# Optimization experiments

Measured on AMD Instinct MI355X. Metric: run time of the kernel, lower is better.

## Reference

```python
import jax, jax.numpy as jnp
import numpy as np

IB = 8      # input/hidden activation bits
ABMVM = 8   # gate activation bits after MVM
ABNM = 8    # near-memory compute bits
NL = 0.05   # analog noise level
CY_DIV = 2.0
CY_SCALE = 2.0


def quant_pass(x, wb, sign):
    # Faithful port of QuantFunc.forward: clip/clamp then fake-quant (round to grid).
    if wb is None or wb == 0:
        return x
    if sign:
        delta = 0.0 if wb == 1 else 1.0 / (2.0 ** (wb - 1))
        x = jnp.clip(x, -1.0 + delta, 1.0 - delta)
    else:
        x = jnp.clip(x, 0.0, 1.0)
    if wb == 1:
        return jnp.sign(x)
    scale = 2.0 ** (wb - 1) if sign else 2.0 ** wb
    return jnp.round(x * scale) / scale


def setup_inputs() -> dict:
    key = jax.random.key(0)
    ks = jax.random.split(key, 7)
    B, I, H = 4096, 1024, 1024
    return {
        "input": jax.random.normal(ks[0], (B, I), jnp.float32),
        "hx": jax.random.normal(ks[1], (B, H), jnp.float32),
        "cx": jax.random.normal(ks[2], (B, H), jnp.float32),
        "weight_ih": jax.random.normal(ks[3], (4 * H, I), jnp.float32) * 0.1,
        "weight_hh": jax.random.normal(ks[4], (4 * H, H), jnp.float32) * 0.1,
        "bias_ih": jax.random.normal(ks[5], (4 * H,), jnp.float32) * 0.1,
        "bias_hh": jax.random.normal(ks[6], (4 * H,), jnp.float32) * 0.1,
        "train": 0,
    }


def reference(input, hx, cx, weight_ih, weight_hh, bias_ih, bias_hh, train):
    # Per-call Gaussian noise (simulated analog hardware); fixed key for reproducibility.
    nk = jax.random.split(jax.random.key(42), 4)
    noise_w_ih = jax.random.normal(nk[0], weight_ih.T.shape, weight_ih.dtype) * weight_ih.max() * NL
    noise_w_hh = jax.random.normal(nk[1], weight_hh.T.shape, weight_hh.dtype) * weight_hh.max() * NL
    noise_b_ih = jax.random.normal(nk[2], bias_ih.shape, bias_ih.dtype) * bias_ih.max() * NL
    noise_b_hh = jax.random.normal(nk[3], bias_hh.shape, bias_hh.dtype) * bias_hh.max() * NL

    # gates: [B, 4H]
    gates = (quant_pass(input, IB, True) @ (weight_ih.T + noise_w_ih) + bias_ih + noise_b_ih
             + quant_pass(hx, IB, True) @ (weight_hh.T + noise_w_hh) + bias_hh + noise_b_hh)

    ingate, forgetgate, cellgate, outgate = jnp.split(gates, 4, axis=1)
    ingate = quant_pass(jax.nn.sigmoid(ingate), ABMVM, False)
    forgetgate = quant_pass(jax.nn.sigmoid(forgetgate), ABMVM, False)
    cellgate = quant_pass(jnp.tanh(cellgate), ABMVM, True)
    outgate = quant_pass(jax.nn.sigmoid(outgate), ABMVM, False)

    cy = quant_pass((quant_pass(forgetgate * cx, ABNM, True)
                     + quant_pass(ingate * cellgate, ABNM, True)) / CY_DIV, ABNM, True)
    hy = quant_pass(outgate * quant_pass(jnp.tanh(cy * CY_SCALE), ABNM, True), ABNM, True)
    return (hy, cy)
```

## Files before the change

### kernel.cpp

```cpp
#include <hip/hip_runtime.h>
#include <hip/hip_bf16.h>
#include <stdint.h>
#include <stddef.h>


#define PART 1

typedef __attribute__((ext_vector_type(8))) short bf16x8;
typedef __attribute__((ext_vector_type(4))) float f32x4;

#define BATCH 4096

#define WS_A_OFF    ((size_t)0)
#define WS_B_OFF    ((size_t)16 << 20)
#define WS_BIAS_OFF ((size_t)48 << 20)
#define WS_MAX_OFF  (WS_BIAS_OFF + 16384)

__host__ __device__ inline void tf2x32(uint32_t k0, uint32_t k1,
                                       uint32_t x0, uint32_t x1,
                                       uint32_t &o0, uint32_t &o1)
{
  const uint32_t k2 = k0 ^ k1 ^ 0x1BD11BDAu;
#define TFR(r) { x0 += x1; x1 = (x1 << (r)) | (x1 >> (32 - (r))); x1 ^= x0; }
  x0 += k0; x1 += k1;
  TFR(13) TFR(15) TFR(26) TFR(6)
  x0 += k1; x1 += k2 + 1u;
  TFR(17) TFR(29) TFR(16) TFR(24)
  x0 += k2; x1 += k0 + 2u;
  TFR(13) TFR(15) TFR(26) TFR(6)
  x0 += k0; x1 += k1 + 3u;
  TFR(17) TFR(29) TFR(16) TFR(24)
  x0 += k1; x1 += k2 + 4u;
  TFR(13) TFR(15) TFR(26) TFR(6)
  x0 += k2; x1 += k0 + 5u;
#undef TFR
  o0 = x0; o1 = x1;
}

__device__ inline uint32_t jax_bits32(uint32_t k0, uint32_t k1, uint32_t i, uint32_t size)
{
#if PART
  uint32_t a, b;
  tf2x32(k0, k1, 0u, i, a, b);
  return a ^ b;
#else
  uint32_t half = size >> 1, a, b;
  if (i < half) { tf2x32(k0, k1, i, i + half, a, b); return a; }
  tf2x32(k0, k1, i - half, i, a, b); return b;
#endif
}

__device__ inline float bits_to_normal(uint32_t bits)
{
  float f = __uint_as_float((bits >> 9) | 0x3F800000u) - 1.0f;
  const float lo = -0x1.fffffep-1f;
  float u = fmaxf(lo, f * 2.0f + lo);
  float w = -log1pf(-u * u);
  float p;
  if (w < 5.0f) {
    w -= 2.5f;
    p = 2.81022636e-08f;
    p = fmaf(p, w, 3.43273939e-07f);
    p = fmaf(p, w, -3.5233877e-06f);
    p = fmaf(p, w, -4.39150654e-06f);
    p = fmaf(p, w, 0.00021858087f);
    p = fmaf(p, w, -0.00125372503f);
    p = fmaf(p, w, -0.00417768164f);
    p = fmaf(p, w, 0.246640727f);
    p = fmaf(p, w, 1.50140941f);
  } else {
    w = sqrtf(w) - 3.0f;
    p = -0.000200214257f;
    p = fmaf(p, w, 0.000100950558f);
    p = fmaf(p, w, 0.00134934322f);
    p = fmaf(p, w, -0.00367342844f);
    p = fmaf(p, w, 0.00573950773f);
    p = fmaf(p, w, -0.0076224613f);
    p = fmaf(p, w, 0.00943887047f);
    p = fmaf(p, w, 1.00167406f);
    p = fmaf(p, w, 2.83297682f);
  }
  return 0x1.6a09e6p+0f * (p * u);
}

__device__ inline float quantS8(float x)
{
  x = fminf(fmaxf(x, -0.9921875f), 0.9921875f);
  return rintf(x * 128.0f) * 0.0078125f;
}
__device__ inline float quantU8(float x)
{
  x = fminf(fmaxf(x, 0.0f), 1.0f);
  return rintf(x * 256.0f) * 0.00390625f;
}
__device__ inline float sigmoid_xla(float x) { return 0.5f + 0.5f * tanhf(0.5f * x); }

__device__ inline unsigned short f2bf(float x)
{
  uint32_t b = __float_as_uint(x);
  return (unsigned short)((b + 0x7FFFu + ((b >> 16) & 1u)) >> 16);
}
__device__ inline float bf2f(unsigned short u) { return __uint_as_float(((uint32_t)u) << 16); }

__device__ inline float dec_max(uint32_t u)
{
  uint32_t bits = (u & 0x80000000u) ? (u ^ 0x80000000u) : ~u;
  return __uint_as_float(bits);
}

__global__ void init_max(uint32_t* mx)
{
  if (threadIdx.x < 4) mx[threadIdx.x] = 0u;
}

__global__ void kmax_all(const float4* __restrict__ wih, const float4* __restrict__ whh,
                         const float4* __restrict__ bih, const float4* __restrict__ bhh,
                         uint32_t* __restrict__ mx)
{
  const int blk = blockIdx.x;
  const float4* src; int n4, bl, nb; uint32_t* out;
  if (blk < 1024)      { src = wih; n4 = 1048576; bl = blk;        nb = 1024; out = mx + 0; }
  else if (blk < 2048) { src = whh; n4 = 1048576; bl = blk - 1024; nb = 1024; out = mx + 1; }
  else if (blk < 2052) { src = bih; n4 = 1024;    bl = blk - 2048; nb = 4;    out = mx + 2; }
  else                 { src = bhh; n4 = 1024;    bl = blk - 2052; nb = 4;    out = mx + 3; }

  float m = -3.4e38f;
  for (int i = bl * 256 + threadIdx.x; i < n4; i += nb * 256) {
    float4 v = src[i];
    m = fmaxf(fmaxf(m, fmaxf(v.x, v.y)), fmaxf(v.z, v.w));
  }
  for (int off = 32; off; off >>= 1) m = fmaxf(m, __shfl_down(m, off, 64));
  __shared__ float sm[4];
  if ((threadIdx.x & 63) == 0) sm[threadIdx.x >> 6] = m;
  __syncthreads();
  if (threadIdx.x == 0) {
    float bm = fmaxf(fmaxf(sm[0], sm[1]), fmaxf(sm[2], sm[3]));
    uint32_t bits = __float_as_uint(bm);
    uint32_t enc = (bits & 0x80000000u) ? ~bits : (bits | 0x80000000u);
    atomicMax(out, enc);
  }
}

__global__ void build_all(const float* __restrict__ wih, const float* __restrict__ whh,
                          const float4* __restrict__ in, const float4* __restrict__ hxp,
                          const float* __restrict__ bih, const float* __restrict__ bhh,
                          unsigned short* __restrict__ A, unsigned short* __restrict__ B,
                          float* __restrict__ biasE, const uint32_t* __restrict__ mxenc,
                          uint32_t kih0, uint32_t kih1, uint32_t khh0, uint32_t khh1,
                          uint32_t kbi0, uint32_t kbi1, uint32_t kbh0, uint32_t kbh1)
{
  const uint32_t blk = blockIdx.x;
  if (blk < 32768u) {
    uint32_t t = blk * 256u + threadIdx.x;
    uint32_t arr = t >> 22;
    uint32_t r = t & 4194303u;
    uint32_t k = r & 1023u;
    uint32_t n = r >> 10;
    const float* w = arr ? whh : wih;
    float mx = dec_max(mxenc[arr]);
    uint32_t key0 = arr ? khh0 : kih0, key1 = arr ? khh1 : kih1;
    uint32_t i = k * 4096u + n;
    float nrm = bits_to_normal(jax_bits32(key0, key1, i, 4194304u));
    float weff = w[(size_t)n * 1024u + k] + (nrm * mx) * 0.05f;
    unsigned short hi = f2bf(weff);
    unsigned short lob = f2bf(weff - bf2f(hi));
    uint32_t np = (n & 1023u) * 4u + (n >> 10);
    size_t base = (size_t)np * 4096u + (arr ? 1024u : 0u) + k;
    B[base] = hi;
    B[base + 2048u] = lob;
  } else if (blk < 40960u) {
    int t = (int)(blk - 32768u) * 256 + threadIdx.x;
    int b = t >> 9;
    int kq = t & 511;
    float4 v = (kq < 256) ? in[b * 256 + kq] : hxp[b * 256 + (kq - 256)];
    unsigned short o[4];
    o[0] = f2bf(quantS8(v.x)); o[1] = f2bf(quantS8(v.y));
    o[2] = f2bf(quantS8(v.z)); o[3] = f2bf(quantS8(v.w));
    *reinterpret_cast<uint64_t*>(A + (size_t)t * 4) = *reinterpret_cast<uint64_t*>(o);
  } else {
    uint32_t j = (blk - 40960u) * 256u + threadIdx.x;
    float mi = dec_max(mxenc[2]), mh = dec_max(mxenc[3]);
    float ni = (bits_to_normal(jax_bits32(kbi0, kbi1, j, 4096u)) * mi) * 0.05f;
    float nh = (bits_to_normal(jax_bits32(kbh0, kbh1, j, 4096u)) * mh) * 0.05f;
    biasE[(j & 1023u) * 4u + (j >> 10)] = ((bih[j] + ni) + bhh[j]) + nh;
  }
}

__device__ __forceinline__ void gload_lds16(const void* g, void* l)
{
  __builtin_amdgcn_global_load_lds((__attribute__((address_space(1))) void*)g,
                                   (__attribute__((address_space(3))) void*)l, 16, 0, 0);
}

#define VM0  asm volatile("s_waitcnt vmcnt(0)" ::: "memory")
#define NOVM
#define SBAR __builtin_amdgcn_s_barrier()
#define SCB  __builtin_amdgcn_sched_barrier(0)

#define BUFSZ 49152

#define TILE_ONE(t_, DO_STAGE_, VM_ASM_)                                          \
  {                                                                               \
    const int buf_ = (t_) & 1;                                                    \
    const unsigned char* pa_  = lds + buf_ * BUFSZ + aoff;                        \
    const unsigned char* pbh_ = lds + buf_ * BUFSZ + 16384 + boffU;               \
    const unsigned char* pbl_ = lds + buf_ * BUFSZ + 32768 + boffU;               \
    bf16x8 bh_[4], bl_[4], afL_[4], afH_[4];                                      \
                 \
    _Pragma("unroll") for (int n_ = 0; n_ < 4; ++n_)                              \
      bh_[n_] = *(const bf16x8*)(pbh_ + n_ * 1024);                               \
    _Pragma("unroll") for (int m_ = 0; m_ < 4; ++m_)                              \
      afL_[m_] = *(const bf16x8*)(pa_ + m_ * 1024);                               \
    if (DO_STAGE_) {                                                              \
      const int ts_ = (t_) + 1;                                                   \
      unsigned char* la_ = lds + (ts_ & 1) * BUFSZ;                               \
      const int ka_ = ts_ * 32;                                                   \
      gload_lds16(Ar0 + ka_, la_ + tid * 16);                                     \
      gload_lds16(Ar1 + ka_, la_ + 8192 + tid * 16);                              \
      gload_lds16(Br0 + ka_, la_ + 16384 + tid * 16);                             \
      gload_lds16(Br1 + ka_, la_ + 16384 + 8192 + tid * 16);                      \
      gload_lds16(Br0 + 2048 + ka_, la_ + 32768 + tid * 16);                      \
      gload_lds16(Br1 + 2048 + ka_, la_ + 32768 + 8192 + tid * 16);               \
    }                                                                             \
    SBAR; SCB;                                                                    \
    __builtin_amdgcn_s_setprio(1);                                                \
    _Pragma("unroll") for (int m_ = 0; m_ < 4; ++m_)                              \
      _Pragma("unroll") for (int n_ = 0; n_ < 4; ++n_)                            \
        acc[m_][n_] = __builtin_amdgcn_mfma_f32_16x16x32_bf16(afL_[m_], bh_[n_],  \
                                                              acc[m_][n_], 0, 0, 0); \
    __builtin_amdgcn_s_setprio(0);                                                \
    SBAR; SCB;                                                                    \
                                                       \
    _Pragma("unroll") for (int m_ = 0; m_ < 4; ++m_)                              \
      afH_[m_] = *(const bf16x8*)(pa_ + (4 + m_) * 1024);                         \
    SBAR; SCB;                                                                    \
    __builtin_amdgcn_s_setprio(1);                                                \
    _Pragma("unroll") for (int m_ = 0; m_ < 4; ++m_)                              \
      _Pragma("unroll") for (int n_ = 0; n_ < 4; ++n_)                            \
        acc[4 + m_][n_] = __builtin_amdgcn_mfma_f32_16x16x32_bf16(afH_[m_], bh_[n_], \
                                                              acc[4 + m_][n_], 0, 0, 0); \
    __builtin_amdgcn_s_setprio(0);                                                \
    SBAR; SCB;                                                                    \
                         \
    _Pragma("unroll") for (int n_ = 0; n_ < 4; ++n_)                              \
      bl_[n_] = *(const bf16x8*)(pbl_ + n_ * 1024);                               \
    SBAR; SCB;                                                                    \
    __builtin_amdgcn_s_setprio(1);                                                \
    _Pragma("unroll") for (int m_ = 0; m_ < 4; ++m_)                              \
      _Pragma("unroll") for (int n_ = 0; n_ < 4; ++n_)                            \
        acc[m_][n_] = __builtin_amdgcn_mfma_f32_16x16x32_bf16(afL_[m_], bl_[n_],  \
                                                              acc[m_][n_], 0, 0, 0); \
    _Pragma("unroll") for (int m_ = 0; m_ < 4; ++m_)                              \
      _Pragma("unroll") for (int n_ = 0; n_ < 4; ++n_)                            \
        acc[4 + m_][n_] = __builtin_amdgcn_mfma_f32_16x16x32_bf16(afH_[m_], bl_[n_], \
                                                              acc[4 + m_][n_], 0, 0, 0); \
    __builtin_amdgcn_s_setprio(0);                                                \
    VM_ASM_;                                                                      \
    SBAR; SCB;                                                                    \
  }

#define LTS 272

__global__ __launch_bounds__(512, 2) void gemm_gates(
    const unsigned short* __restrict__ A,
    const unsigned short* __restrict__ B,
    const float* __restrict__ bias,
    const float* __restrict__ cx,
    float* __restrict__ hy,
    float* __restrict__ cy)
{
  extern __shared__ unsigned char lds[];
  const int tid  = threadIdx.x;
  const int lane = tid & 63;
  const int wave = tid >> 6;
  const int wr = wave >> 2;
  const int wc = wave & 3;

  const int bid = blockIdx.x;
  const int wg  = (bid & 7) * 32 + (bid >> 3);
  const int brow = (wg & 15) * 256;
  const int bcol = (wg >> 4) * 256;

  int sr0, sk0, sr1, sk1;
  {
    int c = tid, p = c >> 3, lc = (c & 7) ^ (p & 7);
    sr0 = p * 2 + (lc >> 2); sk0 = (lc & 3) * 8;
    c = tid + 512; p = c >> 3; lc = (c & 7) ^ (p & 7);
    sr1 = p * 2 + (lc >> 2); sk1 = (lc & 3) * 8;
  }
  const unsigned short* Ar0 = A + (size_t)(brow + sr0) * 2048 + sk0;
  const unsigned short* Ar1 = A + (size_t)(brow + sr1) * 2048 + sk1;
  const unsigned short* Br0 = B + (size_t)(bcol + sr0) * 4096 + sk0;
  const unsigned short* Br1 = B + (size_t)(bcol + sr1) * 4096 + sk1;

  const int lrh = (lane & 15) >> 1;
  const int chk = ((((lane & 1) << 2) | (lane >> 4)) ^ lrh);
  const int aoff  = wr * 8192 + lrh * 128 + chk * 16;
  const int boffU = wc * 4096 + lrh * 128 + chk * 16;

  f32x4 acc[8][4] = {};

  gload_lds16(Ar0, lds + tid * 16);
  gload_lds16(Ar1, lds + 8192 + tid * 16);
  gload_lds16(Br0, lds + 16384 + tid * 16);
  gload_lds16(Br1, lds + 16384 + 8192 + tid * 16);
  gload_lds16(Br0 + 2048, lds + 32768 + tid * 16);
  gload_lds16(Br1 + 2048, lds + 32768 + 8192 + tid * 16);
  VM0;
  SBAR; SCB;

#pragma unroll 1
  for (int t = 0; t < 63; ++t) {
    TILE_ONE(t, 1, VM0);
  }
  TILE_ONE(63, 0, NOVM);

  float* LT = (float*)lds;
  const int col_local0 = wc * 64 + (lane & 15);
  const int lrow = (lane >> 4) << 2;
  const int h = tid & 63;
  const int hg = (bcol >> 2) + h;

#pragma unroll
  for (int hh = 0; hh < 2; ++hh) {
    __syncthreads();
#pragma unroll
    for (int m = 0; m < 4; ++m) {
#pragma unroll
      for (int n = 0; n < 4; ++n) {
        const int cl = col_local0 + n * 16;
        const float bv = bias[bcol + cl];
        const int lr0 = wr * 64 + m * 16 + lrow;
#pragma unroll
        for (int r = 0; r < 4; ++r)
          LT[(lr0 + r) * LTS + cl] = acc[hh * 4 + m][n][r] + bv;
      }
    }
    __syncthreads();
#pragma unroll
    for (int i = 0; i < 16; ++i) {
      const int lr = (tid >> 6) * 16 + i;
      const int grow = brow + ((lr >> 6) << 7) + hh * 64 + (lr & 63);
      const float4 q = *(const float4*)(LT + lr * LTS + 4 * h);
      const size_t oidx = (size_t)grow * 1024 + hg;
      float ing = quantU8(sigmoid_xla(q.x));
      float fg  = quantU8(sigmoid_xla(q.y));
      float cg  = quantS8(tanhf(q.z));
      float og  = quantU8(sigmoid_xla(q.w));
      float c0  = cx[oidx];
      float cyv = quantS8((quantS8(fg * c0) + quantS8(ing * cg)) * 0.5f);
      float hyv = quantS8(og * quantS8(tanhf(cyv * 2.0f)));
      hy[oidx] = hyv;
      cy[oidx] = cyv;
    }
  }
}

extern "C" void kernel_launch(void* const* d_in, const int* in_sizes, int n_in,
                              void* d_out, int out_size, void* d_ws, size_t ws_size,
                              hipStream_t stream)
{
  const float* input = (const float*)d_in[0];
  const float* hx    = (const float*)d_in[1];
  const float* cx    = (const float*)d_in[2];
  const float* wih   = (const float*)d_in[3];
  const float* whh   = (const float*)d_in[4];
  const float* bih   = (const float*)d_in[5];
  const float* bhh   = (const float*)d_in[6];
  (void)in_sizes; (void)n_in; (void)ws_size;

  uint8_t* ws = (uint8_t*)d_ws;
  unsigned short* A   = (unsigned short*)(ws + WS_A_OFF);
  unsigned short* B   = (unsigned short*)(ws + WS_B_OFF);
  float* biasE        = (float*)(ws + WS_BIAS_OFF);
  uint32_t* mx        = (uint32_t*)(ws + WS_MAX_OFF);

  uint32_t nk[4][2];
#if PART
  for (int i = 0; i < 4; ++i) tf2x32(0u, 42u, 0u, (uint32_t)i, nk[i][0], nk[i][1]);
#else
  {
    uint32_t w0[4], w1[4];
    for (int i = 0; i < 4; ++i) tf2x32(0u, 42u, (uint32_t)i, (uint32_t)(i + 4), w0[i], w1[i]);
    uint32_t out8[8] = {w0[0], w0[1], w0[2], w0[3], w1[0], w1[1], w1[2], w1[3]};
    for (int i = 0; i < 4; ++i) { nk[i][0] = out8[2 * i]; nk[i][1] = out8[2 * i + 1]; }
  }
#endif

  init_max<<<1, 64, 0, stream>>>(mx);
  kmax_all<<<2056, 256, 0, stream>>>((const float4*)wih, (const float4*)whh,
                                     (const float4*)bih, (const float4*)bhh, mx);
  build_all<<<40976, 256, 0, stream>>>(wih, whh, (const float4*)input, (const float4*)hx,
                                       bih, bhh, A, B, biasE, mx,
                                       nk[0][0], nk[0][1], nk[1][0], nk[1][1],
                                       nk[2][0], nk[2][1], nk[3][0], nk[3][1]);

  float* hy = (float*)d_out;
  float* cyp = hy + (size_t)BATCH * 1024;

  (void)hipFuncSetAttribute((const void*)gemm_gates,
                            hipFuncAttributeMaxDynamicSharedMemorySize, 139264);
  gemm_gates<<<dim3(256), dim3(512), 139264, stream>>>(A, B, biasE, cx, hy, cyp);
}
```

Before: 214.9 us.

## Triple-buffer GEMM LDS staging with split prefetch and fast sigmoid/tanh

Moves the GEMM main loop from double to triple buffering in LDS. Tiles are prefetched two steps ahead, the global-to-LDS loads are split into A, B-high and B-low groups placed between MFMA phases, and the wait is relaxed to vmcnt(6) so loads overlap compute more. The epilogue's tanhf-based sigmoid and tanh are replaced with exp2/rcp approximations, which may shift the 8-bit quantization boundaries slightly. Dynamic LDS grows to fit the third buffer.

```diff
diff --git a/kernel.cpp b/kernel.cpp
--- a/kernel.cpp
+++ b/kernel.cpp
@@ -93,7 +93,20 @@
   x = fminf(fmaxf(x, 0.0f), 1.0f);
   return rintf(x * 256.0f) * 0.00390625f;
 }
-__device__ inline float sigmoid_xla(float x) { return 0.5f + 0.5f * tanhf(0.5f * x); }
+
+#define LOG2E 1.44269504088896340736f
+__device__ inline float sigmoid_fast(float x)
+{
+  float e = __builtin_amdgcn_exp2f(x * -LOG2E);
+  return __builtin_amdgcn_rcpf(1.0f + e);
+}
+__device__ inline float tanh_fast(float x)
+{
+  float a = fabsf(x);
+  float e = __builtin_amdgcn_exp2f(a * (-2.0f * LOG2E));
+  float t = (1.0f - e) * __builtin_amdgcn_rcpf(1.0f + e);
+  return copysignf(t, x);
+}
 
 __device__ inline unsigned short f2bf(float x)
 {
@@ -192,6 +205,7 @@
                                    (__attribute__((address_space(3))) void*)l, 16, 0, 0);
 }
 
+#define VM6  asm volatile("s_waitcnt vmcnt(6)" ::: "memory")
 #define VM0  asm volatile("s_waitcnt vmcnt(0)" ::: "memory")
 #define NOVM
 #define SBAR __builtin_amdgcn_s_barrier()
@@ -199,29 +213,30 @@
 
 #define BUFSZ 49152
 
-#define TILE_ONE(t_, DO_STAGE_, VM_ASM_)                                          \
+#define STAGE_A(ts_, bi_)                                                         \
+    { unsigned char* la_ = lds + (bi_) * BUFSZ; const int ka_ = (ts_) * 32;       \
+      gload_lds16(Ar0 + ka_, la_ + tid * 16);                                     \
+      gload_lds16(Ar1 + ka_, la_ + 8192 + tid * 16); }
+#define STAGE_BH(ts_, bi_)                                                        \
+    { unsigned char* la_ = lds + (bi_) * BUFSZ; const int ka_ = (ts_) * 32;       \
+      gload_lds16(Br0 + ka_, la_ + 16384 + tid * 16);                             \
+      gload_lds16(Br1 + ka_, la_ + 16384 + 8192 + tid * 16); }
+#define STAGE_BL(ts_, bi_)                                                        \
+    { unsigned char* la_ = lds + (bi_) * BUFSZ; const int ka_ = (ts_) * 32;       \
+      gload_lds16(Br0 + 2048 + ka_, la_ + 32768 + tid * 16);                      \
+      gload_lds16(Br1 + 2048 + ka_, la_ + 32768 + 8192 + tid * 16); }
+
+#define TILE_ONE(t_, BUF_, BUFN_, DO_STAGE_, VM_ASM_)                             \
   {                                                                               \
-    const int buf_ = (t_) & 1;                                                    \
-    const unsigned char* pa_  = lds + buf_ * BUFSZ + aoff;                        \
-    const unsigned char* pbh_ = lds + buf_ * BUFSZ + 16384 + boffU;               \
-    const unsigned char* pbl_ = lds + buf_ * BUFSZ + 32768 + boffU;               \
+    const unsigned char* pa_  = lds + (BUF_) * BUFSZ + aoff;                      \
+    const unsigned char* pbh_ = lds + (BUF_) * BUFSZ + 16384 + boffU;             \
+    const unsigned char* pbl_ = lds + (BUF_) * BUFSZ + 32768 + boffU;             \
     bf16x8 bh_[4], bl_[4], afL_[4], afH_[4];                                      \
-                 \
     _Pragma("unroll") for (int n_ = 0; n_ < 4; ++n_)                              \
       bh_[n_] = *(const bf16x8*)(pbh_ + n_ * 1024);                               \
     _Pragma("unroll") for (int m_ = 0; m_ < 4; ++m_)                              \
       afL_[m_] = *(const bf16x8*)(pa_ + m_ * 1024);                               \
-    if (DO_STAGE_) {                                                              \
-      const int ts_ = (t_) + 1;                                                   \
-      unsigned char* la_ = lds + (ts_ & 1) * BUFSZ;                               \
-      const int ka_ = ts_ * 32;                                                   \
-      gload_lds16(Ar0 + ka_, la_ + tid * 16);                                     \
-      gload_lds16(Ar1 + ka_, la_ + 8192 + tid * 16);                              \
-      gload_lds16(Br0 + ka_, la_ + 16384 + tid * 16);                             \
-      gload_lds16(Br1 + ka_, la_ + 16384 + 8192 + tid * 16);                      \
-      gload_lds16(Br0 + 2048 + ka_, la_ + 32768 + tid * 16);                      \
-      gload_lds16(Br1 + 2048 + ka_, la_ + 32768 + 8192 + tid * 16);               \
-    }                                                                             \
+    if (DO_STAGE_) STAGE_A((t_) + 2, BUFN_);                                      \
     SBAR; SCB;                                                                    \
     __builtin_amdgcn_s_setprio(1);                                                \
     _Pragma("unroll") for (int m_ = 0; m_ < 4; ++m_)                              \
@@ -230,9 +245,9 @@
                                                               acc[m_][n_], 0, 0, 0); \
     __builtin_amdgcn_s_setprio(0);                                                \
     SBAR; SCB;                                                                    \
-                                                       \
     _Pragma("unroll") for (int m_ = 0; m_ < 4; ++m_)                              \
       afH_[m_] = *(const bf16x8*)(pa_ + (4 + m_) * 1024);                         \
+    if (DO_STAGE_) STAGE_BH((t_) + 2, BUFN_);                                     \
     SBAR; SCB;                                                                    \
     __builtin_amdgcn_s_setprio(1);                                                \
     _Pragma("unroll") for (int m_ = 0; m_ < 4; ++m_)                              \
@@ -241,9 +256,9 @@
                                                               acc[4 + m_][n_], 0, 0, 0); \
     __builtin_amdgcn_s_setprio(0);                                                \
     SBAR; SCB;                                                                    \
-                         \
     _Pragma("unroll") for (int n_ = 0; n_ < 4; ++n_)                              \
       bl_[n_] = *(const bf16x8*)(pbl_ + n_ * 1024);                               \
+    if (DO_STAGE_) STAGE_BL((t_) + 2, BUFN_);                                     \
     SBAR; SCB;                                                                    \
     __builtin_amdgcn_s_setprio(1);                                                \
     _Pragma("unroll") for (int m_ = 0; m_ < 4; ++m_)                              \
@@ -300,20 +315,21 @@
 
   f32x4 acc[8][4] = {};
 
-  gload_lds16(Ar0, lds + tid * 16);
-  gload_lds16(Ar1, lds + 8192 + tid * 16);
-  gload_lds16(Br0, lds + 16384 + tid * 16);
-  gload_lds16(Br1, lds + 16384 + 8192 + tid * 16);
-  gload_lds16(Br0 + 2048, lds + 32768 + tid * 16);
-  gload_lds16(Br1 + 2048, lds + 32768 + 8192 + tid * 16);
-  VM0;
+  STAGE_A(0, 0); STAGE_BH(0, 0); STAGE_BL(0, 0);
+  STAGE_A(1, 1); STAGE_BH(1, 1); STAGE_BL(1, 1);
+  VM6;
   SBAR; SCB;
 
 #pragma unroll 1
-  for (int t = 0; t < 63; ++t) {
-    TILE_ONE(t, 1, VM0);
-  }
-  TILE_ONE(63, 0, NOVM);
+  for (int tt = 0; tt < 60; tt += 3) {
+    TILE_ONE(tt + 0, 0, 2, 1, VM6);
+    TILE_ONE(tt + 1, 1, 0, 1, VM6);
+    TILE_ONE(tt + 2, 2, 1, 1, VM6);
+  }
+  TILE_ONE(60, 0, 2, 1, VM6);
+  TILE_ONE(61, 1, 0, 1, VM6);
+  TILE_ONE(62, 2, 0, 0, VM0);
+  TILE_ONE(63, 0, 0, 0, NOVM);
 
   float* LT = (float*)lds;
   const int col_local0 = wc * 64 + (lane & 15);
@@ -343,13 +359,13 @@
       const int grow = brow + ((lr >> 6) << 7) + hh * 64 + (lr & 63);
       const float4 q = *(const float4*)(LT + lr * LTS + 4 * h);
       const size_t oidx = (size_t)grow * 1024 + hg;
-      float ing = quantU8(sigmoid_xla(q.x));
-      float fg  = quantU8(sigmoid_xla(q.y));
-      float cg  = quantS8(tanhf(q.z));
-      float og  = quantU8(sigmoid_xla(q.w));
+      float ing = quantU8(sigmoid_fast(q.x));
+      float fg  = quantU8(sigmoid_fast(q.y));
+      float cg  = quantS8(tanh_fast(q.z));
+      float og  = quantU8(sigmoid_fast(q.w));
       float c0  = cx[oidx];
       float cyv = quantS8((quantS8(fg * c0) + quantS8(ing * cg)) * 0.5f);
-      float hyv = quantS8(og * quantS8(tanhf(cyv * 2.0f)));
+      float hyv = quantS8(og * quantS8(tanh_fast(cyv * 2.0f)));
       hy[oidx] = hyv;
       cy[oidx] = cyv;
     }
@@ -399,6 +415,6 @@
   float* cyp = hy + (size_t)BATCH * 1024;
 
   (void)hipFuncSetAttribute((const void*)gemm_gates,
-                            hipFuncAttributeMaxDynamicSharedMemorySize, 139264);
-  gemm_gates<<<dim3(256), dim3(512), 139264, stream>>>(A, B, biasE, cx, hy, cyp);
-}
+                            hipFuncAttributeMaxDynamicSharedMemorySize, 147456);
+  gemm_gates<<<dim3(256), dim3(512), 147456, stream>>>(A, B, biasE, cx, hy, cyp);
+}
```

Result: faster. 190.5 us (-11.3%).
